# Kernel tuning notes

Hardware: AMD Instinct MI355X
Metric: run time of the kernel (lower is better)

## Reference

```python
import jax, jax.numpy as jnp
import numpy as np

B, T, D, H = 32, 1024, 128, 4
DH = D // H  # per-head dim = 32
NEG = -(2.0**32) + 1.0  # padding value used by SoftmaxWeightedSum
LN_EPS = 1e-9


def setup_inputs() -> dict:
    key = jax.random.key(0)
    k1, k2, k3, k4 = jax.random.split(key, 4)
    x = jax.random.normal(k1, (B, T, D), dtype=jnp.float32)
    keys_length = jax.random.randint(k2, (B, 1), 1, T + 1, dtype=jnp.int32)
    W = jax.random.normal(k3, (D, 3 * D), dtype=jnp.float32) * 0.05
    W_output = jax.random.normal(k4, (D, D), dtype=jnp.float32) * 0.05
    gamma = jnp.ones((D,), dtype=jnp.float32)
    beta = jnp.zeros((D,), dtype=jnp.float32)
    return {"x": x, "keys_length": keys_length, "W": W,
            "W_output": W_output, "gamma": gamma, "beta": beta}


def reference(x, keys_length, W, W_output, gamma, beta):
    # QKV projection: [B,T,D] @ [D,3D] -> [B,T,3D]
    qkv = jnp.einsum('btd,de->bte', x, W)
    q, k, v = jnp.split(qkv, 3, axis=-1)

    # tf.split(axis=2)+concat(axis=0) == head-major [H,B,T,DH]
    def to_heads(t):
        return t.reshape(B, T, H, DH).transpose(2, 0, 1, 3)
    q, k, v = to_heads(q), to_heads(k), to_heads(v)

    # DotAttention with scale by sqrt(per-head key dim)
    scores = jnp.einsum('hbqd,hbkd->hbqk', q, k) / jnp.sqrt(jnp.float32(DH))

    # key padding mask from sequence lengths: [B,T] bool
    key_mask = jnp.arange(T)[None, :] < keys_length  # keys_length is [B,1]
    # causal (future_binding) lower-triangular mask: [T,T]
    causal = jnp.tril(jnp.ones((T, T), dtype=bool))
    mask = causal[None, None, :, :] & key_mask[None, :, None, :]  # [1,B,T,T] -> broadcast over H
    scores = jnp.where(mask, scores, NEG)

    attn = jax.nn.softmax(scores, axis=-1)  # [H,B,T,T]
    out = jnp.einsum('hbqk,hbkd->hbqd', attn, v)  # [H,B,T,DH]

    # concat heads back to channel dim: [B,T,D]
    out = out.transpose(1, 2, 0, 3).reshape(B, T, D)
    out = jnp.einsum('btd,de->bte', out, W_output)

    # residual + layernorm (dropout is identity at inference)
    out = out + x
    mean = jnp.mean(out, axis=-1, keepdims=True)
    var = jnp.var(out, axis=-1, keepdims=True)
    out = (out - mean) * jax.lax.rsqrt(var + LN_EPS) * gamma + beta
    return out
```

## Files before the change

kernel.cpp:

```cpp
#include <hip/hip_runtime.h>
#include <hip/hip_bf16.h>

#define B_ 32
#define T_ 1024
#define D_ 128
#define H_ 4
#define DH_ 32

typedef unsigned short ushort_t;
typedef unsigned int uint_t;
typedef unsigned short ushort4_t __attribute__((ext_vector_type(4)));
typedef unsigned short ushort8_t __attribute__((ext_vector_type(8)));
typedef short short8_t __attribute__((ext_vector_type(8)));
typedef float float4_t __attribute__((ext_vector_type(4)));

__device__ __forceinline__ ushort_t f2bf_bits(float f) {
    __hip_bfloat16 h = __float2bfloat16(f);
    return *reinterpret_cast<ushort_t*>(&h);
}
__device__ __forceinline__ uint_t pk_bf16(float hi, float lo) {
    return __builtin_amdgcn_perm(__float_as_uint(hi), __float_as_uint(lo),
                                 0x07060302u);
}
#if __has_builtin(__builtin_amdgcn_exp2f)
__device__ __forceinline__ float fast_exp2(float x) { return __builtin_amdgcn_exp2f(x); }
#else
__device__ __forceinline__ float fast_exp2(float x) { return exp2f(x); }
#endif

__global__ __launch_bounds__(256) void transpose_weights(
    const float* __restrict__ W, const float* __restrict__ Wo,
    ushort_t* __restrict__ Wt, ushort_t* __restrict__ Wot)
{
    const int id = blockIdx.x * 256 + threadIdx.x;
    if (id < 128 * 384) {
        const int n = id >> 7, k = id & 127;
        Wt[id] = f2bf_bits(W[(size_t)k * 384 + n]);
    } else {
        const int id2 = id - 128 * 384;
        const int n = id2 >> 7, k = id2 & 127;
        Wot[id2] = f2bf_bits(Wo[(size_t)k * 128 + n]);
    }
}

__global__ __launch_bounds__(256) void qkv_mfma(
    const float* __restrict__ x, const ushort_t* __restrict__ Wt,
    __hip_bfloat16* __restrict__ qws, __hip_bfloat16* __restrict__ kws,
    __hip_bfloat16* __restrict__ vtws)
{
    __shared__ ushort_t qkA[2][16 * 200];
    __shared__ ushort_t qkB[2][16 * 72];

    const int tid = threadIdx.x;
    const int lane = tid & 63;
    const int i15 = lane & 15, quad = lane >> 4;
    const int wid = tid >> 6;
    const int wpart = wid & 1;
    const int pairIdx = wid >> 1;
    const int gw = blockIdx.x * 4 + wid;
    const int row0 = (gw >> 1) * 32;

    short8_t af[2][4];
    #pragma unroll
    for (int rg = 0; rg < 2; ++rg) {
        #pragma unroll
        for (int kc = 0; kc < 4; ++kc) {
            const float4 x0 = *(const float4*)(x + (size_t)(row0 + rg * 16 + i15) * 128 + kc * 32 + quad * 8);
            const float4 x1 = *(const float4*)(x + (size_t)(row0 + rg * 16 + i15) * 128 + kc * 32 + quad * 8 + 4);
            short8_t a;
            a[0] = (short)f2bf_bits(x0.x); a[1] = (short)f2bf_bits(x0.y);
            a[2] = (short)f2bf_bits(x0.z); a[3] = (short)f2bf_bits(x0.w);
            a[4] = (short)f2bf_bits(x1.x); a[5] = (short)f2bf_bits(x1.y);
            a[6] = (short)f2bf_bits(x1.z); a[7] = (short)f2bf_bits(x1.w);
            af[rg][kc] = a;
        }
    }

    float4_t acc[2][12];
    #pragma unroll
    for (int rg = 0; rg < 2; ++rg)
        #pragma unroll
        for (int nt = 0; nt < 12; ++nt) acc[rg][nt] = (float4_t){0.f, 0.f, 0.f, 0.f};

    #pragma unroll
    for (int nt = 0; nt < 12; ++nt) {
        const int n = wpart * 192 + nt * 16 + i15;
        const ushort_t* wb = Wt + (size_t)n * 128 + quad * 8;
        #pragma unroll
        for (int kc = 0; kc < 4; ++kc) {
            const short8_t bf = *(const short8_t*)(wb + kc * 32);
            acc[0][nt] = __builtin_amdgcn_mfma_f32_16x16x32_bf16(af[0][kc], bf, acc[0][nt], 0, 0, 0);
            acc[1][nt] = __builtin_amdgcn_mfma_f32_16x16x32_bf16(af[1][kc], bf, acc[1][nt], 0, 0, 0);
        }
    }

    const float scale = 0.17677669529663687f * 1.4426950408889634f;
    const int t = lane >> 2, c4 = lane & 3;

    #pragma unroll
    for (int rg = 0; rg < 2; ++rg) {
        const int r0 = row0 + rg * 16;
        const int b = r0 >> 10, t0 = r0 & 1023;
        if (wpart == 0) {
            ushort_t* Ls = qkA[pairIdx];
            #pragma unroll
            for (int nt = 0; nt < 12; ++nt) {
                const int col = nt * 16 + i15;
                const float sc = (nt < 8) ? scale : 1.f;
                #pragma unroll
                for (int r = 0; r < 4; ++r)
                    Ls[(quad * 4 + r) * 200 + col] = f2bf_bits(acc[rg][nt][r] * sc);
            }
            #pragma unroll
            for (int it = 0; it < 6; ++it) {
                const int col8 = it * 4 + c4;
                const ushort8_t v8 = *(const ushort8_t*)(Ls + t * 200 + col8 * 8);
                __hip_bfloat16* base = (it < 4) ? qws : kws;
                const int h = (it < 4) ? it : (it - 4);
                *(ushort8_t*)((ushort_t*)base +
                    ((size_t)(b * H_ + h) * T_ + t0 + t) * DH_ + c4 * 8) = v8;
            }
        } else {
            ushort_t* Ls = qkB[pairIdx];
            #pragma unroll
            for (int nt = 0; nt < 12; ++nt) {
                if (nt < 4) {
                    const int col = nt * 16 + i15;
                    #pragma unroll
                    for (int r = 0; r < 4; ++r)
                        Ls[(quad * 4 + r) * 72 + col] = f2bf_bits(acc[rg][nt][r]);
                } else {
                    const int ch = nt * 16 + i15 - 64;
                    const int h = ch >> 5, dh = ch & 31;
                    ushort4_t pk;
                    #pragma unroll
                    for (int r = 0; r < 4; ++r) pk[r] = f2bf_bits(acc[rg][nt][r]);
                    *(ushort4_t*)((ushort_t*)vtws +
                        ((size_t)(b * H_ + h) * DH_ + dh) * T_ + t0 + quad * 4) = pk;
                }
            }
            #pragma unroll
            for (int it = 0; it < 2; ++it) {
                const int col8 = it * 4 + c4;
                const ushort8_t v8 = *(const ushort8_t*)(Ls + t * 72 + col8 * 8);
                *(ushort8_t*)((ushort_t*)kws +
                    ((size_t)(b * H_ + 2 + it) * T_ + t0 + t) * DH_ + c4 * 8) = v8;
            }
        }
    }
}

__global__ __launch_bounds__(256) void attn_proj_ln(
    const ushort_t* __restrict__ qws, const ushort_t* __restrict__ kws,
    const ushort_t* __restrict__ vtws, const int* __restrict__ keys_length,
    const ushort_t* __restrict__ Wot, const float* __restrict__ x,
    const float* __restrict__ gamma, const float* __restrict__ beta,
    float* __restrict__ out)
{
    __shared__ ushort_t plds[4][32 * 72];
    __shared__ ushort_t att[32 * 128];

    const int wid = threadIdx.x >> 6;
    const int lane = threadIdx.x & 63;
    const int i15 = lane & 15, quad = lane >> 4;
    const int b = blockIdx.x & 31;
    const int st = 31 - (blockIdx.x >> 5);
    const int qbase = st * 32;
    const int h = wid;
    const int bh = b * 4 + h;
    const int len = keys_length[b];

    const ushort_t* Qb = qws + (size_t)bh * T_ * DH_;
    const ushort_t* Kb = kws + (size_t)bh * T_ * DH_;
    const ushort_t* Vtb = vtws + (size_t)bh * DH_ * T_;

    const short8_t qfA = *(const short8_t*)(Qb + (size_t)(qbase + i15) * DH_ + quad * 8);
    const short8_t qfB = *(const short8_t*)(Qb + (size_t)(qbase + 16 + i15) * DH_ + quad * 8);

    const int kend    = min(qbase + 32, len);
    const int nch     = (kend + 63) >> 6;
    const int limAmax = min(qbase + 16, len);
    const int nfullA  = min(qbase + 1, len) >> 6;
    const int nfullB  = min(qbase + 17, len) >> 6;
    const int limA    = min(qbase + i15 + 1, len);
    const int limB    = min(qbase + 16 + i15 + 1, len);

    ushort_t* pl = plds[h];

    float4_t oA0 = {0,0,0,0}, oA1 = {0,0,0,0}, oB0 = {0,0,0,0}, oB1 = {0,0,0,0};
    float laccA = 0.f, laccB = 0.f;
    const float4_t zero = {0,0,0,0};

    for (int c = 0; c < nch; ++c) {
        const int k0 = c * 64;
        const bool doA = (k0 < limAmax);

        short8_t kf[4], vf[4];
        #pragma unroll
        for (int g = 0; g < 4; ++g)
            kf[g] = *(const short8_t*)(Kb + (size_t)(k0 + g * 16 + i15) * DH_ + quad * 8);
        vf[0] = *(const short8_t*)(Vtb + (size_t)i15 * T_ + k0 + quad * 8);
        vf[1] = *(const short8_t*)(Vtb + (size_t)i15 * T_ + k0 + 32 + quad * 8);
        vf[2] = *(const short8_t*)(Vtb + (size_t)(16 + i15) * T_ + k0 + quad * 8);
        vf[3] = *(const short8_t*)(Vtb + (size_t)(16 + i15) * T_ + k0 + 32 + quad * 8);

        float4_t sB[4], sA[4];
        #pragma unroll
        for (int g = 0; g < 4; ++g)
            sB[g] = __builtin_amdgcn_mfma_f32_16x16x32_bf16(kf[g], qfB, zero, 0, 0, 0);
        if (doA) {
            #pragma unroll
            for (int g = 0; g < 4; ++g)
                sA[g] = __builtin_amdgcn_mfma_f32_16x16x32_bf16(kf[g], qfA, zero, 0, 0, 0);
        }

        {
            const bool fullB = (c < nfullB);
            ushort_t* prow = pl + (16 + i15) * 72 + quad * 4;
            #pragma unroll
            for (int g = 0; g < 4; ++g) {
                float p0 = fast_exp2(sB[g][0]), p1 = fast_exp2(sB[g][1]);
                float p2 = fast_exp2(sB[g][2]), p3 = fast_exp2(sB[g][3]);
                if (!fullB) {
                    const int d = limB - (k0 + g * 16 + quad * 4);
                    p0 = (d > 0) ? p0 : 0.f; p1 = (d > 1) ? p1 : 0.f;
                    p2 = (d > 2) ? p2 : 0.f; p3 = (d > 3) ? p3 : 0.f;
                }
                laccB += (p0 + p1) + (p2 + p3);
                uint2 w; w.x = pk_bf16(p1, p0); w.y = pk_bf16(p3, p2);
                *(uint2*)(prow + g * 16) = w;
            }
        }
        if (doA) {
            const bool fullA = (c < nfullA);
            ushort_t* prow = pl + i15 * 72 + quad * 4;
            #pragma unroll
            for (int g = 0; g < 4; ++g) {
                float p0 = fast_exp2(sA[g][0]), p1 = fast_exp2(sA[g][1]);
                float p2 = fast_exp2(sA[g][2]), p3 = fast_exp2(sA[g][3]);
                if (!fullA) {
                    const int d = limA - (k0 + g * 16 + quad * 4);
                    p0 = (d > 0) ? p0 : 0.f; p1 = (d > 1) ? p1 : 0.f;
                    p2 = (d > 2) ? p2 : 0.f; p3 = (d > 3) ? p3 : 0.f;
                }
                laccA += (p0 + p1) + (p2 + p3);
                uint2 w; w.x = pk_bf16(p1, p0); w.y = pk_bf16(p3, p2);
                *(uint2*)(prow + g * 16) = w;
            }
        }

        {
            const short8_t pfB0 = *(const short8_t*)(pl + (16 + i15) * 72 + quad * 8);
            const short8_t pfB1 = *(const short8_t*)(pl + (16 + i15) * 72 + 32 + quad * 8);
            oB0 = __builtin_amdgcn_mfma_f32_16x16x32_bf16(pfB0, vf[0], oB0, 0, 0, 0);
            oB0 = __builtin_amdgcn_mfma_f32_16x16x32_bf16(pfB1, vf[1], oB0, 0, 0, 0);
            oB1 = __builtin_amdgcn_mfma_f32_16x16x32_bf16(pfB0, vf[2], oB1, 0, 0, 0);
            oB1 = __builtin_amdgcn_mfma_f32_16x16x32_bf16(pfB1, vf[3], oB1, 0, 0, 0);
        }
        if (doA) {
            const short8_t pfA0 = *(const short8_t*)(pl + i15 * 72 + quad * 8);
            const short8_t pfA1 = *(const short8_t*)(pl + i15 * 72 + 32 + quad * 8);
            oA0 = __builtin_amdgcn_mfma_f32_16x16x32_bf16(pfA0, vf[0], oA0, 0, 0, 0);
            oA0 = __builtin_amdgcn_mfma_f32_16x16x32_bf16(pfA1, vf[1], oA0, 0, 0, 0);
            oA1 = __builtin_amdgcn_mfma_f32_16x16x32_bf16(pfA0, vf[2], oA1, 0, 0, 0);
            oA1 = __builtin_amdgcn_mfma_f32_16x16x32_bf16(pfA1, vf[3], oA1, 0, 0, 0);
        }
    }

    laccA += __shfl_xor(laccA, 16, 64); laccA += __shfl_xor(laccA, 32, 64);
    laccB += __shfl_xor(laccB, 16, 64); laccB += __shfl_xor(laccB, 32, 64);

    #pragma unroll
    for (int r = 0; r < 4; ++r) {
        const int q = quad * 4 + r;
        const float invA = 1.f / __shfl(laccA, q, 64);
        const float invB = 1.f / __shfl(laccB, q, 64);
        const int colL = h * 32 + i15, colH = h * 32 + 16 + i15;
        char* ab = (char*)att;
        *(ushort_t*)(ab + ((q * 256 + colL * 2) ^ ((q & 7) << 4)))        = f2bf_bits(oA0[r] * invA);
        *(ushort_t*)(ab + ((q * 256 + colH * 2) ^ ((q & 7) << 4)))        = f2bf_bits(oA1[r] * invA);
        *(ushort_t*)(ab + (((16 + q) * 256 + colL * 2) ^ ((q & 7) << 4))) = f2bf_bits(oB0[r] * invB);
        *(ushort_t*)(ab + (((16 + q) * 256 + colH * 2) ^ ((q & 7) << 4))) = f2bf_bits(oB1[r] * invB);
    }
    __syncthreads();

    if (wid < 2) {
        const int lr = wid * 16 + i15;
        short8_t af[4];
        #pragma unroll
        for (int kc = 0; kc < 4; ++kc)
            af[kc] = *(const short8_t*)((const char*)att +
                ((lr * 256 + kc * 64 + quad * 16) ^ ((lr & 7) << 4)));

        float4_t acc[8];
        #pragma unroll
        for (int nt = 0; nt < 8; ++nt) acc[nt] = (float4_t){0.f, 0.f, 0.f, 0.f};

        #pragma unroll
        for (int nt = 0; nt < 8; ++nt) {
            const ushort_t* wb = Wot + (size_t)(nt * 16 + i15) * 128 + quad * 8;
            #pragma unroll
            for (int kc = 0; kc < 4; ++kc) {
                const short8_t bf = *(const short8_t*)(wb + kc * 32);
                acc[nt] = __builtin_amdgcn_mfma_f32_16x16x32_bf16(af[kc], bf, acc[nt], 0, 0, 0);
            }
        }

        float g[8], be[8];
        #pragma unroll
        for (int nt = 0; nt < 8; ++nt) {
            g[nt] = gamma[nt * 16 + i15];
            be[nt] = beta[nt * 16 + i15];
        }

        const int m0 = b * T_ + qbase + wid * 16;
        #pragma unroll
        for (int r = 0; r < 4; ++r) {
            const int m = m0 + quad * 4 + r;
            float y[8];
            float s1 = 0.f, s2 = 0.f;
            #pragma unroll
            for (int nt = 0; nt < 8; ++nt) {
                y[nt] = acc[nt][r] + x[(size_t)m * 128 + nt * 16 + i15];
                s1 += y[nt];
                s2 += y[nt] * y[nt];
            }
            #pragma unroll
            for (int off = 1; off < 16; off <<= 1) {
                s1 += __shfl_xor(s1, off, 64);
                s2 += __shfl_xor(s2, off, 64);
            }
            const float mean = s1 * (1.f / 128.f);
            const float var = s2 * (1.f / 128.f) - mean * mean;
            const float rstd = rsqrtf(var + 1e-9f);
            #pragma unroll
            for (int nt = 0; nt < 8; ++nt)
                out[(size_t)m * 128 + nt * 16 + i15] = (y[nt] - mean) * rstd * g[nt] + be[nt];
        }
    }
}

extern "C" void kernel_launch(void* const* d_in, const int* in_sizes, int n_in,
                              void* d_out, int out_size, void* d_ws, size_t ws_size,
                              hipStream_t stream) {
    const float* x      = (const float*)d_in[0];
    const int* keys_len = (const int*)d_in[1];
    const float* W      = (const float*)d_in[2];
    const float* Wo     = (const float*)d_in[3];
    const float* gamma  = (const float*)d_in[4];
    const float* beta   = (const float*)d_in[5];
    float* out          = (float*)d_out;

    const size_t seg = (size_t)B_ * H_ * T_ * DH_;
    __hip_bfloat16* qws  = (__hip_bfloat16*)d_ws;
    __hip_bfloat16* kws  = qws + seg;
    __hip_bfloat16* vtws = qws + 2 * seg;
    ushort_t* Wt  = (ushort_t*)(qws + 3 * seg);
    ushort_t* Wot = Wt + 128 * 384;

    transpose_weights<<<256, 256, 0, stream>>>(W, Wo, Wt, Wot);
    qkv_mfma<<<B_ * T_ / 64, 256, 0, stream>>>(x, Wt, qws, kws, vtws);
    attn_proj_ln<<<B_ * (T_ / 32), 256, 0, stream>>>(
        (const ushort_t*)qws, (const ushort_t*)kws, (const ushort_t*)vtws,
        keys_len, Wot, x, gamma, beta, out);
}
```

Before: 133.4 us.

## Fold weight transpose into QKV kernel and prefetch next K/V chunk

Removes the separate transpose_weights launch. The QKV kernel now reads fp32 W directly with strided column loads and converts it to bf16 on the fly, and 16 extra blocks transpose Wo for the attention kernel. The attention loop software-pipelines its K/V fragment loads, issuing the next chunk's loads before the current chunk's softmax and PV MFMAs to hide global latency. In exchange, the W loads become uncoalesced strided scalar loads repeated by every block, and the prefetch raises register pressure.

```diff
diff --git a/kernel.cpp b/kernel.cpp
--- a/kernel.cpp
+++ b/kernel.cpp
@@ -28,28 +28,25 @@
 __device__ __forceinline__ float fast_exp2(float x) { return exp2f(x); }
 #endif
 
-__global__ __launch_bounds__(256) void transpose_weights(
-    const float* __restrict__ W, const float* __restrict__ Wo,
-    ushort_t* __restrict__ Wt, ushort_t* __restrict__ Wot)
-{
-    const int id = blockIdx.x * 256 + threadIdx.x;
-    if (id < 128 * 384) {
-        const int n = id >> 7, k = id & 127;
-        Wt[id] = f2bf_bits(W[(size_t)k * 384 + n]);
-    } else {
-        const int id2 = id - 128 * 384;
-        const int n = id2 >> 7, k = id2 & 127;
-        Wot[id2] = f2bf_bits(Wo[(size_t)k * 128 + n]);
-    }
-}
-
 __global__ __launch_bounds__(256) void qkv_mfma(
-    const float* __restrict__ x, const ushort_t* __restrict__ Wt,
+    const float* __restrict__ x, const float* __restrict__ W,
+    const float* __restrict__ Wo,
     __hip_bfloat16* __restrict__ qws, __hip_bfloat16* __restrict__ kws,
-    __hip_bfloat16* __restrict__ vtws)
+    __hip_bfloat16* __restrict__ vtws, ushort_t* __restrict__ Wot)
 {
     __shared__ ushort_t qkA[2][16 * 200];
     __shared__ ushort_t qkB[2][16 * 72];
+
+    if (blockIdx.x >= 512) {
+        const int base = (blockIdx.x - 512) * 1024 + threadIdx.x * 4;
+        #pragma unroll
+        for (int i = 0; i < 4; ++i) {
+            const int id = base + i;
+            const int n = id >> 7, k = id & 127;
+            Wot[id] = f2bf_bits(Wo[(size_t)k * 128 + n]);
+        }
+        return;
+    }
 
     const int tid = threadIdx.x;
     const int lane = tid & 63;
@@ -85,10 +82,13 @@
     #pragma unroll
     for (int nt = 0; nt < 12; ++nt) {
         const int n = wpart * 192 + nt * 16 + i15;
-        const ushort_t* wb = Wt + (size_t)n * 128 + quad * 8;
+        const float* wcol = W + n;
         #pragma unroll
         for (int kc = 0; kc < 4; ++kc) {
-            const short8_t bf = *(const short8_t*)(wb + kc * 32);
+            short8_t bf;
+            #pragma unroll
+            for (int j = 0; j < 8; ++j)
+                bf[j] = (short)f2bf_bits(wcol[(size_t)(kc * 32 + quad * 8 + j) * 384]);
             acc[0][nt] = __builtin_amdgcn_mfma_f32_16x16x32_bf16(af[0][kc], bf, acc[0][nt], 0, 0, 0);
             acc[1][nt] = __builtin_amdgcn_mfma_f32_16x16x32_bf16(af[1][kc], bf, acc[1][nt], 0, 0, 0);
         }
@@ -191,19 +191,21 @@
     float laccA = 0.f, laccB = 0.f;
     const float4_t zero = {0,0,0,0};
 
+    short8_t kf[4], vf[4];
+    {
+        #pragma unroll
+        for (int g = 0; g < 4; ++g)
+            kf[g] = *(const short8_t*)(Kb + (size_t)(g * 16 + i15) * DH_ + quad * 8);
+        vf[0] = *(const short8_t*)(Vtb + (size_t)i15 * T_ + quad * 8);
+        vf[1] = *(const short8_t*)(Vtb + (size_t)i15 * T_ + 32 + quad * 8);
+        vf[2] = *(const short8_t*)(Vtb + (size_t)(16 + i15) * T_ + quad * 8);
+        vf[3] = *(const short8_t*)(Vtb + (size_t)(16 + i15) * T_ + 32 + quad * 8);
+    }
+
     for (int c = 0; c < nch; ++c) {
         const int k0 = c * 64;
         const bool doA = (k0 < limAmax);
 
-        short8_t kf[4], vf[4];
-        #pragma unroll
-        for (int g = 0; g < 4; ++g)
-            kf[g] = *(const short8_t*)(Kb + (size_t)(k0 + g * 16 + i15) * DH_ + quad * 8);
-        vf[0] = *(const short8_t*)(Vtb + (size_t)i15 * T_ + k0 + quad * 8);
-        vf[1] = *(const short8_t*)(Vtb + (size_t)i15 * T_ + k0 + 32 + quad * 8);
-        vf[2] = *(const short8_t*)(Vtb + (size_t)(16 + i15) * T_ + k0 + quad * 8);
-        vf[3] = *(const short8_t*)(Vtb + (size_t)(16 + i15) * T_ + k0 + 32 + quad * 8);
-
         float4_t sB[4], sA[4];
         #pragma unroll
         for (int g = 0; g < 4; ++g)
@@ -212,6 +214,19 @@
             #pragma unroll
             for (int g = 0; g < 4; ++g)
                 sA[g] = __builtin_amdgcn_mfma_f32_16x16x32_bf16(kf[g], qfA, zero, 0, 0, 0);
+        }
+
+        short8_t kf2[4], vf2[4];
+        const int c2 = c + 1;
+        if (c2 < nch) {
+            const int k2 = c2 * 64;
+            #pragma unroll
+            for (int g = 0; g < 4; ++g)
+                kf2[g] = *(const short8_t*)(Kb + (size_t)(k2 + g * 16 + i15) * DH_ + quad * 8);
+            vf2[0] = *(const short8_t*)(Vtb + (size_t)i15 * T_ + k2 + quad * 8);
+            vf2[1] = *(const short8_t*)(Vtb + (size_t)i15 * T_ + k2 + 32 + quad * 8);
+            vf2[2] = *(const short8_t*)(Vtb + (size_t)(16 + i15) * T_ + k2 + quad * 8);
+            vf2[3] = *(const short8_t*)(Vtb + (size_t)(16 + i15) * T_ + k2 + 32 + quad * 8);
         }
 
         {
@@ -265,6 +280,11 @@
             oA1 = __builtin_amdgcn_mfma_f32_16x16x32_bf16(pfA0, vf[2], oA1, 0, 0, 0);
             oA1 = __builtin_amdgcn_mfma_f32_16x16x32_bf16(pfA1, vf[3], oA1, 0, 0, 0);
         }
+
+        if (c2 < nch) {
+            #pragma unroll
+            for (int g = 0; g < 4; ++g) { kf[g] = kf2[g]; vf[g] = vf2[g]; }
+        }
     }
 
     laccA += __shfl_xor(laccA, 16, 64); laccA += __shfl_xor(laccA, 32, 64);
@@ -355,11 +375,9 @@
     __hip_bfloat16* qws  = (__hip_bfloat16*)d_ws;
     __hip_bfloat16* kws  = qws + seg;
     __hip_bfloat16* vtws = qws + 2 * seg;
-    ushort_t* Wt  = (ushort_t*)(qws + 3 * seg);
-    ushort_t* Wot = Wt + 128 * 384;
-
-    transpose_weights<<<256, 256, 0, stream>>>(W, Wo, Wt, Wot);
-    qkv_mfma<<<B_ * T_ / 64, 256, 0, stream>>>(x, Wt, qws, kws, vtws);
+    ushort_t* Wot = (ushort_t*)(qws + 3 * seg);
+
+    qkv_mfma<<<528, 256, 0, stream>>>(x, W, Wo, qws, kws, vtws, Wot);
     attn_proj_ln<<<B_ * (T_ / 32), 256, 0, stream>>>(
         (const ushort_t*)qws, (const ushort_t*)kws, (const ushort_t*)vtws,
         keys_len, Wot, x, gamma, beta, out);
```

Measured after the change: 130.8 us. Within noise of the previous version (-1.9%).
